# Kernel optimization log

Measured on AMD Instinct MI355X. Metric: run time of the kernel, lower is better.

Reference implementation:

```python
import jax, jax.numpy as jnp
import numpy as np

N = 100_000      # nodes
E = 1_600_000    # edges (avg degree 16)
IN_DIM = 256
HID = 128
N_OUT = 2


def _linear_params(key, fan_in, fan_out):
    kw, kb = jax.random.split(key)
    bound = 1.0 / np.sqrt(fan_in)
    W = jax.random.uniform(kw, (fan_in, fan_out), jnp.float32, -bound, bound)
    b = jax.random.uniform(kb, (fan_out,), jnp.float32, -bound, bound)
    return W, b


def setup_inputs() -> dict:
    key = jax.random.key(0)
    ks = jax.random.split(key, 6)
    edge_index = jax.random.randint(ks[0], (2, E), 0, N, dtype=jnp.int64)
    x = jax.random.normal(ks[1], (N, IN_DIM), jnp.float32)
    Wi, bi = _linear_params(ks[2], IN_DIM, HID)   # NodeInitializer.lin
    W1, b1 = _linear_params(ks[3], HID, HID)      # GCNConv 1
    W2, b2 = _linear_params(ks[4], HID, HID)      # GCNConv 2
    Wh, bh = _linear_params(ks[5], HID, N_OUT)    # head
    return {"edge_index": edge_index, "x": x, "Wi": Wi, "bi": bi,
            "W1": W1, "b1": b1, "W2": W2, "b2": b2, "Wh": Wh, "bh": bh}


def reference(edge_index, x, Wi, bi, W1, b1, W2, b2, Wh, bh):
    n = x.shape[0]
    # GCNConv preprocessing: add self-loops, symmetric degree normalization.
    loops = jnp.arange(n, dtype=edge_index.dtype)
    src = jnp.concatenate([edge_index[0], loops])  # message source
    dst = jnp.concatenate([edge_index[1], loops])  # aggregation target
    deg = jax.ops.segment_sum(jnp.ones(src.shape[0], jnp.float32), dst, num_segments=n)
    dinv = jnp.where(deg > 0, deg ** -0.5, 0.0)
    norm = dinv[src] * dinv[dst]                   # [E+N]

    # NodeInitializer: relu(linear(x)); dropout = identity (eval mode)
    h = jax.nn.relu(x @ Wi + bi)

    # Two GCNConv layers (no relu between, matching SimpleGCN.forward)
    for W, b in ((W1, b1), (W2, b2)):
        msg = (h @ W)[src] * norm[:, None]         # gather + normalize, [E+N, HID]
        h = jax.ops.segment_sum(msg, dst, num_segments=n) + b  # scatter-add

    return h @ Wh + bh                             # [N, N_OUT]
```

## Files before the change

kernel.cpp:

```cpp
#include <hip/hip_runtime.h>
#include <hip/hip_bf16.h>

#define N_NODES 100000
#define N_EDGES 1600000
#define DIM_IN  256
#define DIM_H   128

#define NBKT 782
#define CPAD 16
#define EPB  8192
#define NBLK ((N_EDGES + EPB - 1) / EPB)

typedef __attribute__((ext_vector_type(8))) short short8;
typedef __attribute__((ext_vector_type(4))) float f32x4;

__global__ __launch_bounds__(1024) void k_detect(const int* __restrict__ e,
                                                 int* __restrict__ flag) {
  __shared__ int s;
  if (threadIdx.x == 0) s = 0;
  __syncthreads();
  atomicOr(&s, e[2 * threadIdx.x + 1]);
  __syncthreads();
  if (threadIdx.x == 0) *flag = (s == 0) ? 1 : 0;
}

__device__ __forceinline__ int get_src(const int* e, int is64, int i) {
  return is64 ? e[2 * i] : e[i];
}
__device__ __forceinline__ int get_dst(const int* e, int is64, int i) {
  return is64 ? e[2 * (N_EDGES + i)] : e[N_EDGES + i];
}

__global__ __launch_bounds__(256) void k_zero(int* __restrict__ p, int n) {
  int i = blockIdx.x * 256 + threadIdx.x;
  if (i < n) p[i] = 0;
}

__global__ __launch_bounds__(1024)
void k_binc(const int* __restrict__ eidx, const int* __restrict__ flag,
            int* __restrict__ bcnt) {
  __shared__ int hist[NBKT];
  const int t = threadIdx.x;
  const int is64 = *flag;
  for (int i = t; i < NBKT; i += 1024) hist[i] = 0;
  __syncthreads();
#pragma unroll
  for (int j = 0; j < EPB / 1024; ++j) {
    int e = blockIdx.x * EPB + j * 1024 + t;
    if (e < N_EDGES) {
      unsigned s = (unsigned)get_src(eidx, is64, e);
      unsigned d = (unsigned)get_dst(eidx, is64, e);
      if (s < N_NODES && d < N_NODES) atomicAdd(&hist[d >> 7], 1);
    }
  }
  __syncthreads();
  for (int i = t; i < NBKT; i += 1024) {
    int h = hist[i];
    if (h) atomicAdd(&bcnt[i * CPAD], h);
  }
}

__global__ __launch_bounds__(1024)
void k_bscan(int* __restrict__ bcnt, int* __restrict__ bbase) {
  __shared__ int sm[1024];
  int t = threadIdx.x;
  int v = (t < NBKT) ? bcnt[t * CPAD] : 0;
  sm[t] = v;
  __syncthreads();
  for (int d = 1; d < 1024; d <<= 1) {
    int u = (t >= d) ? sm[t - d] : 0;
    __syncthreads();
    sm[t] += u;
    __syncthreads();
  }
  if (t < NBKT) {
    int excl = sm[t] - v;
    bbase[t] = excl;
    bcnt[t * CPAD] = excl;
    if (t == NBKT - 1) bbase[NBKT] = sm[t];
  }
}

__global__ __launch_bounds__(1024)
void k_bin(const int* __restrict__ eidx, const int* __restrict__ flag,
           int* __restrict__ bcnt, unsigned* __restrict__ ebuf) {
  __shared__ int hist[NBKT];
  __shared__ int cur[NBKT];
  const int t = threadIdx.x;
  const int is64 = *flag;
  for (int i = t; i < NBKT; i += 1024) hist[i] = 0;
  unsigned rec[EPB / 1024];
  int bkt[EPB / 1024];
  __syncthreads();
#pragma unroll
  for (int j = 0; j < EPB / 1024; ++j) {
    int e = blockIdx.x * EPB + j * 1024 + t;
    bkt[j] = -1;
    rec[j] = 0;
    if (e < N_EDGES) {
      unsigned s = (unsigned)get_src(eidx, is64, e);
      unsigned d = (unsigned)get_dst(eidx, is64, e);
      if (s < N_NODES && d < N_NODES) {
        bkt[j] = (int)(d >> 7);
        rec[j] = s | ((d & 127u) << 17);
        atomicAdd(&hist[bkt[j]], 1);
      }
    }
  }
  __syncthreads();
  for (int i = t; i < NBKT; i += 1024) {
    int h = hist[i];
    cur[i] = h ? atomicAdd(&bcnt[i * CPAD], h) : 0;
  }
  __syncthreads();
#pragma unroll
  for (int j = 0; j < EPB / 1024; ++j) {
    if (bkt[j] >= 0) {
      int pos = atomicAdd(&cur[bkt[j]], 1);
      ebuf[pos] = rec[j];
    }
  }
}

__global__ __launch_bounds__(256)
void k_csr(const int* __restrict__ bbase, const unsigned* __restrict__ ebuf,
           int* __restrict__ off, float* __restrict__ dinv,
           int* __restrict__ csr) {
  __shared__ int hist[128];
  __shared__ int scn[128];
  __shared__ int cur[128];
  const int b = blockIdx.x, t = threadIdx.x;
  const int n0 = b << 7;
  const int start = bbase[b], end = bbase[b + 1];
  if (t < 128) hist[t] = 0;
  __syncthreads();
  for (int i = start + t; i < end; i += 256) {
    atomicAdd(&hist[ebuf[i] >> 17], 1);
  }
  __syncthreads();
  if (t < 128) scn[t] = hist[t];
  __syncthreads();
  for (int d = 1; d < 128; d <<= 1) {
    int u = (t < 128 && t >= d) ? scn[t - d] : 0;
    __syncthreads();
    if (t < 128) scn[t] += u;
    __syncthreads();
  }
  if (t < 128) {
    int node = n0 + t;
    if (node < N_NODES) {
      off[node] = start + scn[t];
      dinv[node] = rsqrtf(1.0f + (float)hist[t]);
      cur[t] = start + scn[t] - hist[t];
    }
  }
  __syncthreads();
  for (int i = start + t; i < end; i += 256) {
    unsigned r = ebuf[i];
    int pos = atomicAdd(&cur[r >> 17], 1);
    csr[pos] = (int)(r & 0x1FFFFu);
  }
}

__device__ __forceinline__ ushort f2bf(float f) {
  unsigned u = __float_as_uint(f);
  unsigned r = (u + 0x7fffu + ((u >> 16) & 1u)) >> 16;
  return (ushort)r;
}
__device__ __forceinline__ float bf2f(ushort h) {
  return __uint_as_float(((unsigned)h) << 16);
}

__device__ __forceinline__ void load8(const float* p, float* o) {
  float4 a = reinterpret_cast<const float4*>(p)[0];
  float4 b = reinterpret_cast<const float4*>(p)[1];
  o[0] = a.x; o[1] = a.y; o[2] = a.z; o[3] = a.w;
  o[4] = b.x; o[5] = b.y; o[6] = b.z; o[7] = b.w;
}

__global__ __launch_bounds__(256)
void k_bsplit(const float* __restrict__ W, const int CH, ushort* __restrict__ outHi) {
  int idx = blockIdx.x * 256 + threadIdx.x;
  if (idx >= CH * 512) return;
  int n  = idx & 15;
  int qq = (idx >> 4) & 3;
  int nt = (idx >> 6) & 7;
  int c  = idx >> 9;
  int col = nt * 16 + n;
  short8 h8, l8;
#pragma unroll
  for (int j = 0; j < 8; ++j) {
    float v = W[(size_t)(c * 32 + qq * 8 + j) * DIM_H + col];
    ushort hb = f2bf(v);
    ushort lb = f2bf(v - bf2f(hb));
    h8[j] = (short)hb;
    l8[j] = (short)lb;
  }
  ((short8*)outHi)[idx] = h8;
  ((short8*)outHi)[CH * 512 + idx] = l8;
}

__global__ __launch_bounds__(256)
void k_wcc(const float* __restrict__ W1, const float* __restrict__ W2,
           const float* __restrict__ Wh, const float* __restrict__ b1,
           const float* __restrict__ b2, const float* __restrict__ bh,
           float* __restrict__ Wcc) {
  __shared__ float Wc2s[DIM_H][2];
  const int t = threadIdx.x;
  const int i = t >> 1, j = t & 1;
  float s = 0.f;
#pragma unroll 4
  for (int m = 0; m < DIM_H; ++m) s += W2[(size_t)i * DIM_H + m] * Wh[m * 2 + j];
  Wc2s[i][j] = s;
  __syncthreads();
  float c = 0.f;
#pragma unroll 4
  for (int k = 0; k < DIM_H; ++k) c += W1[(size_t)i * DIM_H + k] * Wc2s[k][j];
  Wcc[i * 2 + j] = c;
  if (t < 2) {
    float a = 0.f, b = 0.f;
    for (int k = 0; k < DIM_H; ++k) {
      a += b1[k] * Wc2s[k][t];
      b += b2[k] * Wh[k * 2 + t];
    }
    Wcc[256 + t] = a;
    Wcc[258 + t] = b + bh[t];
  }
}

template <int K>
__global__ __launch_bounds__(256)
void k_gemm_xz(const float* __restrict__ A, const ushort* __restrict__ Bfrag,
               const float* __restrict__ bias, const float* __restrict__ Wcc,
               const float* __restrict__ dinv, float4* __restrict__ tbl) {
  constexpr int CH = K / 32;
  __shared__ __align__(16) ushort AhiS[256 * 8];
  __shared__ __align__(16) ushort AloS[256 * 8];
  __shared__ float zred[2][4][4][4][4];
  const int tid = threadIdx.x;
  const int m0 = blockIdx.x * 64;
  const int wave = tid >> 6, lane = tid & 63;
  const int m_l = lane & 15, quad = lane >> 4;
  const int rs = tid >> 2, q = tid & 3;

  f32x4 acc[2][4];
#pragma unroll
  for (int i = 0; i < 2; ++i)
#pragma unroll
    for (int j = 0; j < 4; ++j) acc[i][j] = (f32x4){0.f, 0.f, 0.f, 0.f};

  const short8* Bhi8 = (const short8*)Bfrag;
  const short8* Blo8 = Bhi8 + CH * 512;
  short8* Ah8 = (short8*)AhiS;
  short8* Al8 = (short8*)AloS;

  for (int c = 0; c < CH; ++c) {
    float v[8];
    const int gm = m0 + rs;
    if (gm < N_NODES) {
      load8(&A[(size_t)gm * K + c * 32 + q * 8], v);
    } else {
#pragma unroll
      for (int j = 0; j < 8; ++j) v[j] = 0.f;
    }
    short8 h8, l8;
#pragma unroll
    for (int j = 0; j < 8; ++j) {
      ushort hb = f2bf(v[j]);
      ushort lb = f2bf(v[j] - bf2f(hb));
      h8[j] = (short)hb;
      l8[j] = (short)lb;
    }
    __syncthreads();
    const int ent = (rs >> 4) * 64 + q * 16 + (rs & 15);
    Ah8[ent] = h8;
    Al8[ent] = l8;
    __syncthreads();

    short8 ahi[4], alo[4];
#pragma unroll
    for (int mt = 0; mt < 4; ++mt) {
      ahi[mt] = Ah8[mt * 64 + quad * 16 + m_l];
      alo[mt] = Al8[mt * 64 + quad * 16 + m_l];
    }
#pragma unroll
    for (int ntl = 0; ntl < 2; ++ntl) {
      const int bent = ((c * 8 + wave * 2 + ntl) * 4 + quad) * 16 + m_l;
      short8 bhi = Bhi8[bent];
      short8 blo = Blo8[bent];
#pragma unroll
      for (int mt = 0; mt < 4; ++mt) {
        acc[ntl][mt] = __builtin_amdgcn_mfma_f32_16x16x32_bf16(ahi[mt], bhi, acc[ntl][mt], 0, 0, 0);
        acc[ntl][mt] = __builtin_amdgcn_mfma_f32_16x16x32_bf16(ahi[mt], blo, acc[ntl][mt], 0, 0, 0);
        acc[ntl][mt] = __builtin_amdgcn_mfma_f32_16x16x32_bf16(alo[mt], bhi, acc[ntl][mt], 0, 0, 0);
      }
    }
  }

  float p0[4][4], p1[4][4];
#pragma unroll
  for (int mt = 0; mt < 4; ++mt)
#pragma unroll
    for (int r = 0; r < 4; ++r) { p0[mt][r] = 0.f; p1[mt][r] = 0.f; }
#pragma unroll
  for (int ntl = 0; ntl < 2; ++ntl) {
    const int colg = (wave * 2 + ntl) * 16 + m_l;
    const float bv = bias[colg];
    const float w0 = Wcc[colg * 2 + 0];
    const float w1 = Wcc[colg * 2 + 1];
#pragma unroll
    for (int mt = 0; mt < 4; ++mt)
#pragma unroll
      for (int r = 0; r < 4; ++r) {
        float hv = fmaxf(acc[ntl][mt][r] + bv, 0.f);
        p0[mt][r] += hv * w0;
        p1[mt][r] += hv * w1;
      }
  }
#pragma unroll
  for (int o = 1; o < 16; o <<= 1) {
#pragma unroll
    for (int mt = 0; mt < 4; ++mt)
#pragma unroll
      for (int r = 0; r < 4; ++r) {
        p0[mt][r] += __shfl_xor(p0[mt][r], o);
        p1[mt][r] += __shfl_xor(p1[mt][r], o);
      }
  }
  if (m_l == 0) {
#pragma unroll
    for (int mt = 0; mt < 4; ++mt)
#pragma unroll
      for (int r = 0; r < 4; ++r) {
        zred[0][wave][quad][mt][r] = p0[mt][r];
        zred[1][wave][quad][mt][r] = p1[mt][r];
      }
  }
  __syncthreads();
  if (tid < 64) {
    const int mt = tid >> 4, qd = (tid >> 2) & 3, r = tid & 3;
    const int rowg = m0 + tid;
    if (rowg < N_NODES) {
      float s0 = zred[0][0][qd][mt][r] + zred[0][1][qd][mt][r] +
                 zred[0][2][qd][mt][r] + zred[0][3][qd][mt][r];
      float s1 = zred[1][0][qd][mt][r] + zred[1][1][qd][mt][r] +
                 zred[1][2][qd][mt][r] + zred[1][3][qd][mt][r];
      float dn = dinv[rowg];
      tbl[rowg] = make_float4(dn * s0, dn * s1, dn, 0.f);
    }
  }
}

__global__ __launch_bounds__(256)
void k_aggr1(const int* __restrict__ off, const int* __restrict__ csr,
             const float4* __restrict__ tbl, float2* __restrict__ tb2,
             float* __restrict__ g) {
  int node = blockIdx.x * 256 + threadIdx.x;
  if (node >= N_NODES) return;
  int start = (node == 0) ? 0 : off[node - 1];
  int end = off[node];
  float4 self = tbl[node];
  float s0 = self.x, s1 = self.y, sd = self.z;
  int e = start;
  for (; e + 3 < end; e += 4) {
    int i0 = csr[e], i1 = csr[e + 1], i2 = csr[e + 2], i3 = csr[e + 3];
    float4 v0 = tbl[i0];
    float4 v1 = tbl[i1];
    float4 v2 = tbl[i2];
    float4 v3 = tbl[i3];
    s0 += (v0.x + v1.x) + (v2.x + v3.x);
    s1 += (v0.y + v1.y) + (v2.y + v3.y);
    sd += (v0.z + v1.z) + (v2.z + v3.z);
  }
  for (; e < end; ++e) {
    float4 v = tbl[csr[e]];
    s0 += v.x; s1 += v.y; sd += v.z;
  }
  float dn = self.z;
  tb2[node] = make_float2(dn * dn * s0, dn * dn * s1);
  g[node] = dn * sd;
}

__global__ __launch_bounds__(256)
void k_aggr2(const int* __restrict__ off, const int* __restrict__ csr,
             const float2* __restrict__ tb2, const float* __restrict__ dinv,
             const float* __restrict__ g, const float* __restrict__ tail,
             float* __restrict__ out) {
  int node = blockIdx.x * 256 + threadIdx.x;
  if (node >= N_NODES) return;
  int start = (node == 0) ? 0 : off[node - 1];
  int end = off[node];
  float2 self = tb2[node];
  float s0 = self.x, s1 = self.y;
  int e = start;
  for (; e + 3 < end; e += 4) {
    int i0 = csr[e], i1 = csr[e + 1], i2 = csr[e + 2], i3 = csr[e + 3];
    float2 v0 = tb2[i0];
    float2 v1 = tb2[i1];
    float2 v2 = tb2[i2];
    float2 v3 = tb2[i3];
    s0 += (v0.x + v1.x) + (v2.x + v3.x);
    s1 += (v0.y + v1.y) + (v2.y + v3.y);
  }
  for (; e < end; ++e) {
    float2 v = tb2[csr[e]];
    s0 += v.x; s1 += v.y;
  }
  float dn = dinv[node], gv = g[node];
  float o0 = dn * s0 + gv * tail[0] + tail[2];
  float o1 = dn * s1 + gv * tail[1] + tail[3];
  reinterpret_cast<float2*>(out)[node] = make_float2(o0, o1);
}

__global__ __launch_bounds__(256) void k_count(const int* __restrict__ eidx,
                                               const int* __restrict__ flag,
                                               int* __restrict__ off) {
  int e = blockIdx.x * 256 + threadIdx.x;
  int is64 = *flag;
  if (e < N_EDGES) {
    unsigned d = (unsigned)get_dst(eidx, is64, e);
    if (d < N_NODES) atomicAdd(&off[d], 1);
  }
}

__global__ __launch_bounds__(256) void k_dinv_old(const int* __restrict__ off,
                                                  float* __restrict__ dinv) {
  int i = blockIdx.x * 256 + threadIdx.x;
  if (i < N_NODES) dinv[i] = rsqrtf(1.0f + (float)off[i]);
}

template <int K>
__global__ __launch_bounds__(256)
void k_gemm(const float* __restrict__ A, const float* __restrict__ B,
            const float* __restrict__ bias, const float* __restrict__ scale,
            float* __restrict__ C, const int do_relu) {
  __shared__ float As[64][33];
  const int tid = threadIdx.x;
  const int tx = tid & 15;
  const int ty = tid >> 4;
  const int m0 = blockIdx.x * 64;

  float acc[4][8];
#pragma unroll
  for (int i = 0; i < 4; ++i)
#pragma unroll
    for (int j = 0; j < 8; ++j) acc[i][j] = 0.f;

  const int rs = tid >> 2;
  const int ks = (tid & 3) * 8;

  for (int k0 = 0; k0 < K; k0 += 32) {
    float av8[8];
    const int gm = m0 + rs;
    if (gm < N_NODES) {
      load8(&A[(size_t)gm * K + k0 + ks], av8);
    } else {
#pragma unroll
      for (int j = 0; j < 8; ++j) av8[j] = 0.f;
    }
    __syncthreads();
#pragma unroll
    for (int j = 0; j < 8; ++j) As[rs][ks + j] = av8[j];
    __syncthreads();

    const float* Bp = B + (size_t)k0 * DIM_H + tx * 8;
#pragma unroll 4
    for (int k = 0; k < 32; ++k) {
      float bv[8];
      load8(Bp + (size_t)k * DIM_H, bv);
      float av[4];
#pragma unroll
      for (int rr = 0; rr < 4; ++rr) av[rr] = As[ty * 4 + rr][k];
#pragma unroll
      for (int rr = 0; rr < 4; ++rr)
#pragma unroll
        for (int cc = 0; cc < 8; ++cc)
          acc[rr][cc] = fmaf(av[rr], bv[cc], acc[rr][cc]);
    }
  }

  float bs[8];
  if (bias) {
    load8(bias + tx * 8, bs);
  } else {
#pragma unroll
    for (int j = 0; j < 8; ++j) bs[j] = 0.f;
  }
#pragma unroll
  for (int rr = 0; rr < 4; ++rr) {
    const int gm = m0 + ty * 4 + rr;
    if (gm < N_NODES) {
      float sc = scale ? scale[gm] : 1.0f;
      float v[8];
#pragma unroll
      for (int cc = 0; cc < 8; ++cc) {
        float t = acc[rr][cc] + bs[cc];
        if (do_relu) t = fmaxf(t, 0.f);
        v[cc] = t * sc;
      }
      float* Cp = &C[(size_t)gm * DIM_H + tx * 8];
      reinterpret_cast<float4*>(Cp)[0] = make_float4(v[0], v[1], v[2], v[3]);
      reinterpret_cast<float4*>(Cp)[1] = make_float4(v[4], v[5], v[6], v[7]);
    }
  }
}

__global__ __launch_bounds__(256)
void k_aggr_init(const float* __restrict__ t, const float* __restrict__ dinv,
                 const float* __restrict__ bias, float* __restrict__ h) {
  int idx = blockIdx.x * 256 + threadIdx.x;
  if (idx < N_NODES * DIM_H) {
    int i = idx >> 7;
    int c = idx & 127;
    float d = dinv[i];
    h[idx] = bias[c] + t[idx] * d * d;
  }
}

__global__ __launch_bounds__(256)
void k_aggr_edges(const int* __restrict__ eidx, const int* __restrict__ flag,
                  const float* __restrict__ t, const float* __restrict__ dinv,
                  float* __restrict__ h) {
  int e = blockIdx.x * 2 + (threadIdx.x >> 7);
  int c = threadIdx.x & 127;
  int is64 = *flag;
  if (e < N_EDGES) {
    unsigned s = (unsigned)get_src(eidx, is64, e);
    unsigned d = (unsigned)get_dst(eidx, is64, e);
    if (s < N_NODES && d < N_NODES) {
      float nrm = dinv[s] * dinv[d];
      unsafeAtomicAdd(&h[(size_t)d * DIM_H + c], t[(size_t)s * DIM_H + c] * nrm);
    }
  }
}

__global__ __launch_bounds__(256)
void k_head_f32(const float* __restrict__ h, const float* __restrict__ Wh,
                const float* __restrict__ bh, float* __restrict__ out) {
  int node = blockIdx.x * 4 + (threadIdx.x >> 6);
  int lane = threadIdx.x & 63;
  if (node >= N_NODES) return;
  float h0 = h[(size_t)node * DIM_H + lane];
  float h1 = h[(size_t)node * DIM_H + 64 + lane];
  float s0 = h0 * Wh[lane * 2 + 0] + h1 * Wh[(lane + 64) * 2 + 0];
  float s1 = h0 * Wh[lane * 2 + 1] + h1 * Wh[(lane + 64) * 2 + 1];
#pragma unroll
  for (int off = 32; off > 0; off >>= 1) {
    s0 += __shfl_down(s0, off);
    s1 += __shfl_down(s1, off);
  }
  if (lane == 0) {
    reinterpret_cast<float2*>(out)[node] = make_float2(s0 + bh[0], s1 + bh[1]);
  }
}

extern "C" void kernel_launch(void* const* d_in, const int* in_sizes, int n_in,
                              void* d_out, int out_size, void* d_ws, size_t ws_size,
                              hipStream_t stream) {
  (void)in_sizes; (void)n_in; (void)out_size;
  const int* eidx = (const int*)d_in[0];
  const float* x  = (const float*)d_in[1];
  const float* Wi = (const float*)d_in[2];
  const float* bi = (const float*)d_in[3];
  const float* W1 = (const float*)d_in[4];
  const float* b1 = (const float*)d_in[5];
  const float* W2 = (const float*)d_in[6];
  const float* b2 = (const float*)d_in[7];
  const float* Wh = (const float*)d_in[8];
  const float* bh = (const float*)d_in[9];
  float* out = (float*)d_out;

  const int gE  = (N_EDGES + 255) / 256;
  const int gM  = (N_NODES + 63) / 64;
  const int gW  = (N_NODES + 3) / 4;
  const int gN256 = (N_NODES + 255) / 256;

  char* ws = (char*)d_ws;
  int* flag = (int*)ws;
  k_detect<<<1, 1024, 0, stream>>>(eidx, flag);

  const size_t need1 = 17410048;

  if (ws_size >= need1) {
    int*      bcnt  = (int*)(ws + 4096);
    int*      bbase = (int*)(ws + 57344);
    float*    Wcc   = (float*)(ws + 61440);
    ushort*   bfWi  = (ushort*)(ws + 65536);
    int*      off   = (int*)(ws + 262144);
    float*    dinv  = (float*)(ws + 720896);
    float*    g     = (float*)(ws + 1179648);
    float4*   tbl   = (float4*)(ws + 1638400);
    float2*   tb2   = (float2*)(ws + 3407872);
    int*      csr   = (int*)(ws + 4456448);
    unsigned* ebuf  = (unsigned*)(ws + 11010048);

    k_zero<<<(NBKT * CPAD + 255) / 256, 256, 0, stream>>>(bcnt, NBKT * CPAD);
    k_binc<<<NBLK, 1024, 0, stream>>>(eidx, flag, bcnt);
    k_bscan<<<1, 1024, 0, stream>>>(bcnt, bbase);
    k_bin<<<NBLK, 1024, 0, stream>>>(eidx, flag, bcnt, ebuf);
    k_csr<<<NBKT, 256, 0, stream>>>(bbase, ebuf, off, dinv, csr);

    k_bsplit<<<16, 256, 0, stream>>>(Wi, 8, bfWi);
    k_wcc<<<1, 256, 0, stream>>>(W1, W2, Wh, b1, b2, bh, Wcc);

    k_gemm_xz<DIM_IN><<<gM, 256, 0, stream>>>(x, bfWi, bi, Wcc, dinv, tbl);
    k_aggr1<<<gN256, 256, 0, stream>>>(off, csr, tbl, tb2, g);
    k_aggr2<<<gN256, 256, 0, stream>>>(off, csr, tb2, dinv, g, Wcc + 256, out);
  } else {
    const int gN  = (N_NODES + 255) / 256;
    int*   off  = (int*)(ws + 4096);
    float* dinv = (float*)(ws + 404480);
    float* fbA  = (float*)(ws + 804864);
    float* fbB  = (float*)(ws + 804864 + (size_t)N_NODES * DIM_H * 4);
    const int gNH = (N_NODES * DIM_H + 255) / 256;
    const int gE2 = (N_EDGES + 1) / 2;
    k_zero<<<gN, 256, 0, stream>>>(off, N_NODES);
    k_count<<<gE, 256, 0, stream>>>(eidx, flag, off);
    k_dinv_old<<<gN, 256, 0, stream>>>(off, dinv);

    k_gemm<DIM_IN><<<gM, 256, 0, stream>>>(x, Wi, bi, nullptr, fbA, 1);
    k_gemm<DIM_H><<<gM, 256, 0, stream>>>(fbA, W1, nullptr, nullptr, fbB, 0);
    k_aggr_init<<<gNH, 256, 0, stream>>>(fbB, dinv, b1, fbA);
    k_aggr_edges<<<gE2, 256, 0, stream>>>(eidx, flag, fbB, dinv, fbA);
    k_gemm<DIM_H><<<gM, 256, 0, stream>>>(fbA, W2, nullptr, nullptr, fbB, 0);
    k_aggr_init<<<gNH, 256, 0, stream>>>(fbB, dinv, b2, fbA);
    k_aggr_edges<<<gE2, 256, 0, stream>>>(eidx, flag, fbB, dinv, fbA);
    k_head_f32<<<gW, 256, 0, stream>>>(fbA, Wh, bh, out);
  }
}
```

Before: 292.0 us.

## Merge small setup kernels and restructure input GEMM to per-wave row tiles

Folds the int64 detection and bucket-count zeroing into one launch, and merges the Wi bf16 split with the collapsed-weight computation into one launch, which cuts the number of tiny kernel launches. The input GEMM is also rewritten so that each wave owns 16 rows across all 128 columns and loads A straight from global memory into registers. This removes the LDS staging, the __syncthreads barriers and the cross-wave shared-memory reduction. In exchange each wave reads all B fragments itself, so B-fragment global/cache traffic per block goes up, and accumulator register use rises.

```diff
diff --git a/kernel.cpp b/kernel.cpp
--- a/kernel.cpp
+++ b/kernel.cpp
@@ -14,21 +14,27 @@
 typedef __attribute__((ext_vector_type(8))) short short8;
 typedef __attribute__((ext_vector_type(4))) float f32x4;
 
-__global__ __launch_bounds__(1024) void k_detect(const int* __restrict__ e,
-                                                 int* __restrict__ flag) {
-  __shared__ int s;
-  if (threadIdx.x == 0) s = 0;
-  __syncthreads();
-  atomicOr(&s, e[2 * threadIdx.x + 1]);
-  __syncthreads();
-  if (threadIdx.x == 0) *flag = (s == 0) ? 1 : 0;
-}
-
 __device__ __forceinline__ int get_src(const int* e, int is64, int i) {
   return is64 ? e[2 * i] : e[i];
 }
 __device__ __forceinline__ int get_dst(const int* e, int is64, int i) {
   return is64 ? e[2 * (N_EDGES + i)] : e[N_EDGES + i];
+}
+
+__global__ __launch_bounds__(1024)
+void k_init(const int* __restrict__ e, int* __restrict__ flag,
+            int* __restrict__ bcnt) {
+  if (blockIdx.x == 0) {
+    __shared__ int s;
+    if (threadIdx.x == 0) s = 0;
+    __syncthreads();
+    atomicOr(&s, e[2 * threadIdx.x + 1]);
+    __syncthreads();
+    if (threadIdx.x == 0) *flag = (s == 0) ? 1 : 0;
+  } else {
+    int i = (blockIdx.x - 1) * 1024 + threadIdx.x;
+    if (i < NBKT * CPAD) bcnt[i] = 0;
+  }
 }
 
 __global__ __launch_bounds__(256) void k_zero(int* __restrict__ p, int n) {
@@ -179,9 +185,37 @@
 }
 
 __global__ __launch_bounds__(256)
-void k_bsplit(const float* __restrict__ W, const int CH, ushort* __restrict__ outHi) {
+void k_prep(const float* __restrict__ Wi, const float* __restrict__ W1,
+            const float* __restrict__ W2, const float* __restrict__ Wh,
+            const float* __restrict__ b1, const float* __restrict__ b2,
+            const float* __restrict__ bh, ushort* __restrict__ outHi,
+            float* __restrict__ Wcc) {
+  __shared__ float Wc2s[DIM_H][2];
+  constexpr int CH = DIM_IN / 32;
+  if (blockIdx.x == 16) {
+    const int t = threadIdx.x;
+    const int i = t >> 1, j = t & 1;
+    float s = 0.f;
+#pragma unroll 4
+    for (int m = 0; m < DIM_H; ++m) s += W2[(size_t)i * DIM_H + m] * Wh[m * 2 + j];
+    Wc2s[i][j] = s;
+    __syncthreads();
+    float c = 0.f;
+#pragma unroll 4
+    for (int k = 0; k < DIM_H; ++k) c += W1[(size_t)i * DIM_H + k] * Wc2s[k][j];
+    Wcc[i * 2 + j] = c;
+    if (t < 2) {
+      float a = 0.f, b = 0.f;
+      for (int k = 0; k < DIM_H; ++k) {
+        a += b1[k] * Wc2s[k][t];
+        b += b2[k] * Wh[k * 2 + t];
+      }
+      Wcc[256 + t] = a;
+      Wcc[258 + t] = b + bh[t];
+    }
+    return;
+  }
   int idx = blockIdx.x * 256 + threadIdx.x;
-  if (idx >= CH * 512) return;
   int n  = idx & 15;
   int qq = (idx >> 4) & 3;
   int nt = (idx >> 6) & 7;
@@ -190,7 +224,7 @@
   short8 h8, l8;
 #pragma unroll
   for (int j = 0; j < 8; ++j) {
-    float v = W[(size_t)(c * 32 + qq * 8 + j) * DIM_H + col];
+    float v = Wi[(size_t)(c * 32 + qq * 8 + j) * DIM_H + col];
     ushort hb = f2bf(v);
     ushort lb = f2bf(v - bf2f(hb));
     h8[j] = (short)hb;
@@ -200,153 +234,82 @@
   ((short8*)outHi)[CH * 512 + idx] = l8;
 }
 
-__global__ __launch_bounds__(256)
-void k_wcc(const float* __restrict__ W1, const float* __restrict__ W2,
-           const float* __restrict__ Wh, const float* __restrict__ b1,
-           const float* __restrict__ b2, const float* __restrict__ bh,
-           float* __restrict__ Wcc) {
-  __shared__ float Wc2s[DIM_H][2];
-  const int t = threadIdx.x;
-  const int i = t >> 1, j = t & 1;
-  float s = 0.f;
-#pragma unroll 4
-  for (int m = 0; m < DIM_H; ++m) s += W2[(size_t)i * DIM_H + m] * Wh[m * 2 + j];
-  Wc2s[i][j] = s;
-  __syncthreads();
-  float c = 0.f;
-#pragma unroll 4
-  for (int k = 0; k < DIM_H; ++k) c += W1[(size_t)i * DIM_H + k] * Wc2s[k][j];
-  Wcc[i * 2 + j] = c;
-  if (t < 2) {
-    float a = 0.f, b = 0.f;
-    for (int k = 0; k < DIM_H; ++k) {
-      a += b1[k] * Wc2s[k][t];
-      b += b2[k] * Wh[k * 2 + t];
-    }
-    Wcc[256 + t] = a;
-    Wcc[258 + t] = b + bh[t];
-  }
-}
-
 template <int K>
 __global__ __launch_bounds__(256)
 void k_gemm_xz(const float* __restrict__ A, const ushort* __restrict__ Bfrag,
                const float* __restrict__ bias, const float* __restrict__ Wcc,
                const float* __restrict__ dinv, float4* __restrict__ tbl) {
   constexpr int CH = K / 32;
-  __shared__ __align__(16) ushort AhiS[256 * 8];
-  __shared__ __align__(16) ushort AloS[256 * 8];
-  __shared__ float zred[2][4][4][4][4];
   const int tid = threadIdx.x;
-  const int m0 = blockIdx.x * 64;
   const int wave = tid >> 6, lane = tid & 63;
   const int m_l = lane & 15, quad = lane >> 4;
-  const int rs = tid >> 2, q = tid & 3;
-
-  f32x4 acc[2][4];
-#pragma unroll
-  for (int i = 0; i < 2; ++i)
-#pragma unroll
-    for (int j = 0; j < 4; ++j) acc[i][j] = (f32x4){0.f, 0.f, 0.f, 0.f};
+  const int mrow = blockIdx.x * 64 + wave * 16;
+
+  f32x4 acc[8];
+#pragma unroll
+  for (int nt = 0; nt < 8; ++nt) acc[nt] = (f32x4){0.f, 0.f, 0.f, 0.f};
 
   const short8* Bhi8 = (const short8*)Bfrag;
   const short8* Blo8 = Bhi8 + CH * 512;
-  short8* Ah8 = (short8*)AhiS;
-  short8* Al8 = (short8*)AloS;
-
+
+  const int rowc = (mrow + m_l < N_NODES) ? (mrow + m_l) : (N_NODES - 1);
+  const float* Ap = &A[(size_t)rowc * K + quad * 8];
+
+#pragma unroll 2
   for (int c = 0; c < CH; ++c) {
     float v[8];
-    const int gm = m0 + rs;
-    if (gm < N_NODES) {
-      load8(&A[(size_t)gm * K + c * 32 + q * 8], v);
-    } else {
-#pragma unroll
-      for (int j = 0; j < 8; ++j) v[j] = 0.f;
-    }
-    short8 h8, l8;
+    load8(Ap + c * 32, v);
+    short8 ahi, alo;
 #pragma unroll
     for (int j = 0; j < 8; ++j) {
       ushort hb = f2bf(v[j]);
       ushort lb = f2bf(v[j] - bf2f(hb));
-      h8[j] = (short)hb;
-      l8[j] = (short)lb;
-    }
-    __syncthreads();
-    const int ent = (rs >> 4) * 64 + q * 16 + (rs & 15);
-    Ah8[ent] = h8;
-    Al8[ent] = l8;
-    __syncthreads();
-
-    short8 ahi[4], alo[4];
-#pragma unroll
-    for (int mt = 0; mt < 4; ++mt) {
-      ahi[mt] = Ah8[mt * 64 + quad * 16 + m_l];
-      alo[mt] = Al8[mt * 64 + quad * 16 + m_l];
-    }
-#pragma unroll
-    for (int ntl = 0; ntl < 2; ++ntl) {
-      const int bent = ((c * 8 + wave * 2 + ntl) * 4 + quad) * 16 + m_l;
+      ahi[j] = (short)hb;
+      alo[j] = (short)lb;
+    }
+#pragma unroll
+    for (int nt = 0; nt < 8; ++nt) {
+      const int bent = ((c * 8 + nt) * 4 + quad) * 16 + m_l;
       short8 bhi = Bhi8[bent];
       short8 blo = Blo8[bent];
-#pragma unroll
-      for (int mt = 0; mt < 4; ++mt) {
-        acc[ntl][mt] = __builtin_amdgcn_mfma_f32_16x16x32_bf16(ahi[mt], bhi, acc[ntl][mt], 0, 0, 0);
-        acc[ntl][mt] = __builtin_amdgcn_mfma_f32_16x16x32_bf16(ahi[mt], blo, acc[ntl][mt], 0, 0, 0);
-        acc[ntl][mt] = __builtin_amdgcn_mfma_f32_16x16x32_bf16(alo[mt], bhi, acc[ntl][mt], 0, 0, 0);
-      }
-    }
-  }
-
-  float p0[4][4], p1[4][4];
-#pragma unroll
-  for (int mt = 0; mt < 4; ++mt)
-#pragma unroll
-    for (int r = 0; r < 4; ++r) { p0[mt][r] = 0.f; p1[mt][r] = 0.f; }
-#pragma unroll
-  for (int ntl = 0; ntl < 2; ++ntl) {
-    const int colg = (wave * 2 + ntl) * 16 + m_l;
+      acc[nt] = __builtin_amdgcn_mfma_f32_16x16x32_bf16(ahi, bhi, acc[nt], 0, 0, 0);
+      acc[nt] = __builtin_amdgcn_mfma_f32_16x16x32_bf16(ahi, blo, acc[nt], 0, 0, 0);
+      acc[nt] = __builtin_amdgcn_mfma_f32_16x16x32_bf16(alo, bhi, acc[nt], 0, 0, 0);
+    }
+  }
+
+  float p0[4], p1[4];
+#pragma unroll
+  for (int r = 0; r < 4; ++r) { p0[r] = 0.f; p1[r] = 0.f; }
+#pragma unroll
+  for (int nt = 0; nt < 8; ++nt) {
+    const int colg = nt * 16 + m_l;
     const float bv = bias[colg];
     const float w0 = Wcc[colg * 2 + 0];
     const float w1 = Wcc[colg * 2 + 1];
 #pragma unroll
-    for (int mt = 0; mt < 4; ++mt)
-#pragma unroll
-      for (int r = 0; r < 4; ++r) {
-        float hv = fmaxf(acc[ntl][mt][r] + bv, 0.f);
-        p0[mt][r] += hv * w0;
-        p1[mt][r] += hv * w1;
+    for (int r = 0; r < 4; ++r) {
+      float hv = fmaxf(acc[nt][r] + bv, 0.f);
+      p0[r] += hv * w0;
+      p1[r] += hv * w1;
+    }
+  }
+#pragma unroll
+  for (int o = 1; o < 16; o <<= 1) {
+#pragma unroll
+    for (int r = 0; r < 4; ++r) {
+      p0[r] += __shfl_xor(p0[r], o);
+      p1[r] += __shfl_xor(p1[r], o);
+    }
+  }
+  if (m_l == 0) {
+#pragma unroll
+    for (int r = 0; r < 4; ++r) {
+      const int rowg = mrow + quad * 4 + r;
+      if (rowg < N_NODES) {
+        float dn = dinv[rowg];
+        tbl[rowg] = make_float4(dn * p0[r], dn * p1[r], dn, 0.f);
       }
-  }
-#pragma unroll
-  for (int o = 1; o < 16; o <<= 1) {
-#pragma unroll
-    for (int mt = 0; mt < 4; ++mt)
-#pragma unroll
-      for (int r = 0; r < 4; ++r) {
-        p0[mt][r] += __shfl_xor(p0[mt][r], o);
-        p1[mt][r] += __shfl_xor(p1[mt][r], o);
-      }
-  }
-  if (m_l == 0) {
-#pragma unroll
-    for (int mt = 0; mt < 4; ++mt)
-#pragma unroll
-      for (int r = 0; r < 4; ++r) {
-        zred[0][wave][quad][mt][r] = p0[mt][r];
-        zred[1][wave][quad][mt][r] = p1[mt][r];
-      }
-  }
-  __syncthreads();
-  if (tid < 64) {
-    const int mt = tid >> 4, qd = (tid >> 2) & 3, r = tid & 3;
-    const int rowg = m0 + tid;
-    if (rowg < N_NODES) {
-      float s0 = zred[0][0][qd][mt][r] + zred[0][1][qd][mt][r] +
-                 zred[0][2][qd][mt][r] + zred[0][3][qd][mt][r];
-      float s1 = zred[1][0][qd][mt][r] + zred[1][1][qd][mt][r] +
-                 zred[1][2][qd][mt][r] + zred[1][3][qd][mt][r];
-      float dn = dinv[rowg];
-      tbl[rowg] = make_float4(dn * s0, dn * s1, dn, 0.f);
     }
   }
 }
@@ -577,7 +540,6 @@
 
   char* ws = (char*)d_ws;
   int* flag = (int*)ws;
-  k_detect<<<1, 1024, 0, stream>>>(eidx, flag);
 
   const size_t need1 = 17410048;
 
@@ -594,14 +556,13 @@
     int*      csr   = (int*)(ws + 4456448);
     unsigned* ebuf  = (unsigned*)(ws + 11010048);
 
-    k_zero<<<(NBKT * CPAD + 255) / 256, 256, 0, stream>>>(bcnt, NBKT * CPAD);
+    k_init<<<1 + (NBKT * CPAD + 1023) / 1024, 1024, 0, stream>>>(eidx, flag, bcnt);
     k_binc<<<NBLK, 1024, 0, stream>>>(eidx, flag, bcnt);
     k_bscan<<<1, 1024, 0, stream>>>(bcnt, bbase);
     k_bin<<<NBLK, 1024, 0, stream>>>(eidx, flag, bcnt, ebuf);
     k_csr<<<NBKT, 256, 0, stream>>>(bbase, ebuf, off, dinv, csr);
 
-    k_bsplit<<<16, 256, 0, stream>>>(Wi, 8, bfWi);
-    k_wcc<<<1, 256, 0, stream>>>(W1, W2, Wh, b1, b2, bh, Wcc);
+    k_prep<<<17, 256, 0, stream>>>(Wi, W1, W2, Wh, b1, b2, bh, bfWi, Wcc);
 
     k_gemm_xz<DIM_IN><<<gM, 256, 0, stream>>>(x, bfWi, bi, Wcc, dinv, tbl);
     k_aggr1<<<gN256, 256, 0, stream>>>(off, csr, tbl, tb2, g);
@@ -614,6 +575,7 @@
     float* fbB  = (float*)(ws + 804864 + (size_t)N_NODES * DIM_H * 4);
     const int gNH = (N_NODES * DIM_H + 255) / 256;
     const int gE2 = (N_EDGES + 1) / 2;
+    k_init<<<1, 1024, 0, stream>>>(eidx, flag, (int*)(ws + 4096));
     k_zero<<<gN, 256, 0, stream>>>(off, N_NODES);
     k_count<<<gE, 256, 0, stream>>>(eidx, flag, off);
     k_dinv_old<<<gN, 256, 0, stream>>>(off, dinv);
```

Result: slower. 302.4 us (+3.5%).
